# Kernel optimization log

Measured on AMD Instinct MI355X. Metric: run time of the kernel, lower is better.

## Reference

```python
import jax, jax.numpy as jnp
import numpy as np
from jax import lax

# Model constants (match init_kwargs)
DIM = 512
NUM_HEADS = 8
HEAD_DIM = 64
INNER = NUM_HEADS * HEAD_DIM  # 512
SCALE = HEAD_DIM ** -0.5
# CoaT ConvRelPosEnc window dict {3:2, 5:3, 7:3}: head-group sizes and kernel sizes
HEAD_SPLITS = [2, 3, 3]
KSIZES = [3, 5, 7]


def _depthwise_conv(x, w, b):
    # x: [B, Cg, H, W], w: [Cg, 1, k, k] (OIHW, depthwise), b: [Cg]
    cg = x.shape[1]
    y = lax.conv_general_dilated(
        x, w, window_strides=(1, 1), padding='SAME',
        feature_group_count=cg,
        dimension_numbers=('NCHW', 'OIHW', 'NCHW'))
    return y + b[None, :, None, None]


def setup_inputs() -> dict:
    key = jax.random.key(0)
    ks = jax.random.split(key, 10)
    B, Himg, Wimg = 16, 56, 56
    N = Himg * Wimg
    x = jax.random.normal(ks[0], (B, N, DIM), dtype=jnp.float32)
    w_qkv = jax.random.normal(ks[1], (3 * INNER, DIM), dtype=jnp.float32) * 0.02
    w_proj = jax.random.normal(ks[2], (DIM, INNER), dtype=jnp.float32) * 0.02
    b_proj = jnp.zeros((DIM,), dtype=jnp.float32)
    # depthwise conv params per head group: channels = split * HEAD_DIM
    w3 = jax.random.normal(ks[3], (2 * HEAD_DIM, 1, 3, 3), dtype=jnp.float32) * 0.02
    b3 = jnp.zeros((2 * HEAD_DIM,), dtype=jnp.float32)
    w5 = jax.random.normal(ks[4], (3 * HEAD_DIM, 1, 5, 5), dtype=jnp.float32) * 0.02
    b5 = jnp.zeros((3 * HEAD_DIM,), dtype=jnp.float32)
    w7 = jax.random.normal(ks[5], (3 * HEAD_DIM, 1, 7, 7), dtype=jnp.float32) * 0.02
    b7 = jnp.zeros((3 * HEAD_DIM,), dtype=jnp.float32)
    return {"x": x, "H": Himg, "W": Wimg,
            "w_qkv": w_qkv, "w_proj": w_proj, "b_proj": b_proj,
            "w3": w3, "b3": b3, "w5": w5, "b5": b5, "w7": w7, "b7": b7}


def reference(x, H, W, w_qkv, w_proj, b_proj, w3, b3, w5, b5, w7, b7):
    B, N, C = x.shape
    h, d = NUM_HEADS, HEAD_DIM
    qkv = x @ w_qkv.T  # [B, N, 3*INNER]
    q, k, v = jnp.split(qkv, 3, axis=-1)
    # b n (h d) -> b h n d
    def to_heads(t):
        return t.reshape(B, N, h, d).transpose(0, 2, 1, 3)
    q, k, v = to_heads(q), to_heads(k), to_heads(v)
    # factorized attention: softmax(k) over sequence dim, then two batched GEMMs
    k_softmax = jax.nn.softmax(k, axis=2)
    kv = jnp.einsum('bhnk,bhnv->bhkv', k_softmax, v)          # [B,h,d,d]
    factor_att = jnp.einsum('bhnk,bhkv->bhnv', q, kv)          # [B,h,N,d]
    # ConvRelPosEnc: depthwise conv on v (as 2D map), elementwise multiply by q
    v_img = v.transpose(0, 1, 3, 2).reshape(B, h * d, H, W)    # [B, h*d, H, W]
    c0, c1 = HEAD_SPLITS[0] * d, (HEAD_SPLITS[0] + HEAD_SPLITS[1]) * d
    conv_v = jnp.concatenate([
        _depthwise_conv(v_img[:, :c0], w3, b3),
        _depthwise_conv(v_img[:, c0:c1], w5, b5),
        _depthwise_conv(v_img[:, c1:], w7, b7),
    ], axis=1)                                                 # [B, h*d, H, W]
    conv_v = conv_v.reshape(B, h, d, N).transpose(0, 1, 3, 2)  # [B,h,N,d]
    crpe = q * conv_v
    out = SCALE * factor_att + crpe                            # [B,h,N,d]
    out = out.transpose(0, 2, 1, 3).reshape(B, N, h * d)       # b h n d -> b n (h d)
    out = out @ w_proj.T + b_proj
    return out
```

## Files before the change

### kernel.cpp

```cpp
#include <hip/hip_runtime.h>
#include <hip/hip_bf16.h>
#include <cstdint>
#include <cstddef>

using u16 = unsigned short;
using u32 = unsigned int;
using f32x4 = __attribute__((ext_vector_type(4))) float;
using bf16x8 = __attribute__((ext_vector_type(8))) short;

#define NB   16
#define NSEQ 3136
#define NH   8
#define HD   64
#define CDIM 512
#define CQKV 1536

static __device__ __forceinline__ u16 f2bf(float f) {
  u32 u = __builtin_bit_cast(u32, f);
  u = (u + 0x7FFFu + ((u >> 16) & 1u)) >> 16;
  return (u16)u;
}
static __device__ __forceinline__ float bf2f(u16 h) {
  u32 u = ((u32)h) << 16;
  return __builtin_bit_cast(float, u);
}
static __device__ __forceinline__ void async16(const void* g, void* l) {
  __builtin_amdgcn_global_load_lds((const __attribute__((address_space(1))) u32*)g,
                                   (__attribute__((address_space(3))) u32*)l, 16, 0, 0);
}

__global__ __launch_bounds__(256) void cvt_kernel(const float* __restrict__ in,
                                                  u16* __restrict__ out, int n4) {
  int i = (int)(blockIdx.x * 256 + threadIdx.x);
  if (i >= n4) return;
  f32x4 v = *(const f32x4*)(in + (size_t)i * 4);
  uint2 uu;
  uu.x = (u32)f2bf(v[0]) | ((u32)f2bf(v[1]) << 16);
  uu.y = (u32)f2bf(v[2]) | ((u32)f2bf(v[3]) << 16);
  *(uint2*)(out + (size_t)i * 4) = uu;
}

#define VMW(n) asm volatile("s_waitcnt vmcnt(" #n ")" ::: "memory")

template<bool OUT_FP32>
__global__ __launch_bounds__(512, 2) void gemm256(
    const u16* __restrict__ Ap, const u16* __restrict__ Bp, void* __restrict__ Cp,
    const float* __restrict__ bias, int K, int lda, int ldb, int ldc, int nbn)
{
  __shared__ u16 sm[2][2][2][128 * 64];
  int nwg = (int)gridDim.x;
  int bid = (int)blockIdx.x;
  int wg = (bid & 7) * (nwg >> 3) + (bid >> 3);
  int bm = wg / nbn, bn = wg - bm * nbn;
  int m0 = bm * 256, n0 = bn * 256;
  int t = (int)threadIdx.x;
  int lane = t & 63, w = t >> 6;
  int wm = w >> 2, wn = w & 3;
  int lr = lane & 15, lk = (lane >> 4) * 8;

  f32x4 acc[2][2][4][2] = {};
  bf16x8 av[4][2], bv[2][2];
  const int KT = K >> 6;

  auto stage = [&](int b, int op, int half, int kt) {
    const u16* P = op ? Bp : Ap;
    int ld = op ? ldb : lda;
    int base0 = op ? n0 : m0;
    int gc = (kt << 6) + ((((t & 7) ^ ((t >> 3) & 7))) << 3);
    #pragma unroll
    for (int rd = 0; rd < 2; ++rd) {
      int gr = base0 + half * 128 + rd * 64 + (t >> 3);
      async16(P + (size_t)gr * ld + gc, &sm[b][op][half][rd * 4096 + w * 512]);
    }
  };
  auto LOADA = [&](int b, int h) {
    #pragma unroll
    for (int mi = 0; mi < 4; ++mi)
      #pragma unroll
      for (int kk = 0; kk < 2; ++kk) {
        int r = wm * 64 + mi * 16 + lr;
        int c = kk * 32 + lk;
        av[mi][kk] = *(const bf16x8*)&sm[b][0][h][r * 64 + (c ^ ((r & 7) << 3))];
      }
  };
  auto LOADB = [&](int b, int g) {
    #pragma unroll
    for (int ni = 0; ni < 2; ++ni)
      #pragma unroll
      for (int kk = 0; kk < 2; ++kk) {
        int r = wn * 32 + ni * 16 + lr;
        int c = kk * 32 + lk;
        bv[ni][kk] = *(const bf16x8*)&sm[b][1][g][r * 64 + (c ^ ((r & 7) << 3))];
      }
  };

#define BARSEQ                                                  \
  __builtin_amdgcn_s_barrier();                                 \
  asm volatile("s_waitcnt lgkmcnt(0)" ::: "memory");            \
  __builtin_amdgcn_sched_barrier(0);                            \
  __builtin_amdgcn_s_setprio(1)
#define ENDP                                                    \
  __builtin_amdgcn_s_setprio(0);                                \
  __builtin_amdgcn_s_barrier()
#define MMQ(h_, g_)                                                          \
  _Pragma("unroll")                                                          \
  for (int kk = 0; kk < 2; ++kk) {                                           \
    _Pragma("unroll")                                                        \
    for (int mi = 0; mi < 4; ++mi) {                                         \
      _Pragma("unroll")                                                      \
      for (int ni = 0; ni < 2; ++ni)                                         \
        acc[h_][g_][mi][ni] = __builtin_amdgcn_mfma_f32_16x16x32_bf16(       \
            av[mi][kk], bv[ni][kk], acc[h_][g_][mi][ni], 0, 0, 0);           \
    }                                                                        \
  }

  stage(0, 0, 0, 0); stage(0, 1, 0, 0); stage(0, 0, 1, 0); stage(0, 1, 1, 0);
  VMW(4);
  __builtin_amdgcn_s_barrier();

  for (int kt = 0; kt < KT - 1; ++kt) {
    int bb = kt & 1;
    LOADA(bb, 0); LOADB(bb, 0);
    stage(bb ^ 1, 0, 0, kt + 1);
    VMW(2);
    BARSEQ; MMQ(0, 0); ENDP;
    LOADB(bb, 1);
    stage(bb ^ 1, 1, 0, kt + 1);
    BARSEQ; MMQ(0, 1); ENDP;
    LOADA(bb, 1);
    stage(bb ^ 1, 0, 1, kt + 1);
    BARSEQ; MMQ(1, 1); ENDP;
    LOADB(bb, 0);
    stage(bb ^ 1, 1, 1, kt + 1);
    VMW(4);
    BARSEQ; MMQ(1, 0); ENDP;
  }
  {
    int bb = (KT - 1) & 1;
    LOADA(bb, 0); LOADB(bb, 0);
    VMW(0);
    BARSEQ; MMQ(0, 0); ENDP;
    LOADB(bb, 1);
    BARSEQ; MMQ(0, 1); ENDP;
    LOADA(bb, 1);
    BARSEQ; MMQ(1, 1); ENDP;
    LOADB(bb, 0);
    BARSEQ; MMQ(1, 0); ENDP;
  }
#undef MMQ
#undef BARSEQ
#undef ENDP

  if constexpr (!OUT_FP32) {
    __syncthreads();
    u16* cs = (u16*)sm;
    #pragma unroll
    for (int h = 0; h < 2; ++h)
      #pragma unroll
      for (int g = 0; g < 2; ++g)
        #pragma unroll
        for (int mi = 0; mi < 4; ++mi)
          #pragma unroll
          for (int ni = 0; ni < 2; ++ni)
            #pragma unroll
            for (int r = 0; r < 4; ++r) {
              int row = h * 128 + wm * 64 + mi * 16 + (lane >> 4) * 4 + r;
              int col = g * 128 + wn * 32 + ni * 16 + lr;
              cs[row * 256 + (col ^ (((row >> 2) & 7) << 3))] = f2bf(acc[h][g][mi][ni][r]);
            }
    __syncthreads();
    #pragma unroll
    for (int i = 0; i < 16; ++i) {
      int e = (i * 512 + t) * 8;
      int row = e >> 8, col = e & 255;
      uint4 v = *(const uint4*)&cs[row * 256 + (col ^ (((row >> 2) & 7) << 3))];
      *(uint4*)&((u16*)Cp)[(size_t)(m0 + row) * ldc + n0 + col] = v;
    }
  } else {
    float* cf = (float*)sm;
    #pragma unroll
    for (int h = 0; h < 2; ++h) {
      __syncthreads();
      #pragma unroll
      for (int g = 0; g < 2; ++g)
        #pragma unroll
        for (int mi = 0; mi < 4; ++mi)
          #pragma unroll
          for (int ni = 0; ni < 2; ++ni)
            #pragma unroll
            for (int r = 0; r < 4; ++r) {
              int row = wm * 64 + mi * 16 + (lane >> 4) * 4 + r;
              int col = g * 128 + wn * 32 + ni * 16 + lr;
              cf[row * 256 + (col ^ (((row >> 2) & 7) << 3))] = acc[h][g][mi][ni][r];
            }
      __syncthreads();
      #pragma unroll
      for (int i = 0; i < 16; ++i) {
        int e = (i * 512 + t) * 4;
        int row = e >> 8, col = e & 255;
        f32x4 v = *(const f32x4*)&cf[row * 256 + (col ^ (((row >> 2) & 7) << 3))];
        f32x4 b4 = *(const f32x4*)&bias[n0 + col];
        v += b4;
        *(f32x4*)&((float*)Cp)[(size_t)(m0 + h * 128 + row) * ldc + n0 + col] = v;
      }
    }
  }
}


static __device__ __forceinline__ void kvp_body(int bid, char* smem,
    const u16* __restrict__ qkvb, float* __restrict__ part) {
  int ns = bid & 7, h = (bid >> 3) & 7, b = bid >> 6;
  int t = (int)threadIdx.x;
  int lane = t & 63, w = t >> 6;
  float* ek = (float*)smem;
  u16*  vv  = (u16*)(smem + 14336);
  float* mg = (float*)(smem + 21504);
  int dk0 = (lane >> 3) * 8, dv0 = (lane & 7) * 8;
  float acc[8][8] = {};
  float sacc = 0.f;
  int nbase = ns * 392;
  for (int c0 = 0; c0 < 392; c0 += 56) {
    __syncthreads();
    for (int idx = t; idx < 448; idx += 256) {
      int row = idx >> 3, c8 = idx & 7;
      size_t go = (size_t)(b * NSEQ + nbase + c0 + row) * CQKV + h * HD + c8 * 8;
      uint4 kq = *(const uint4*)&qkvb[go + CDIM];
      uint4 vq = *(const uint4*)&qkvb[go + 2 * CDIM];
      const u16* kp = (const u16*)&kq;
      #pragma unroll
      for (int j = 0; j < 8; ++j)
        ek[row * 64 + c8 * 8 + j] = __expf(bf2f(kp[j]));
      *(uint4*)&vv[row * 64 + c8 * 8] = vq;
    }
    __syncthreads();
    if (w == 0) {
      #pragma unroll 4
      for (int n = 0; n < 56; ++n) sacc += ek[n * 64 + lane];
    }
    for (int n = w * 14; n < w * 14 + 14; ++n) {
      f32x4 e0 = *(const f32x4*)&ek[n * 64 + dk0];
      f32x4 e1 = *(const f32x4*)&ek[n * 64 + dk0 + 4];
      bf16x8 vq = *(const bf16x8*)&vv[n * 64 + dv0];
      float vf[8];
      #pragma unroll
      for (int j = 0; j < 8; ++j) vf[j] = bf2f((u16)vq[j]);
      #pragma unroll
      for (int i = 0; i < 4; ++i)
        #pragma unroll
        for (int j = 0; j < 8; ++j) {
          acc[i][j]     += e0[i] * vf[j];
          acc[i + 4][j] += e1[i] * vf[j];
        }
    }
  }
  __syncthreads();
  for (int wi = 0; wi < 4; ++wi) {
    if (w == wi) {
      #pragma unroll
      for (int i = 0; i < 8; ++i) {
        #pragma unroll
        for (int j4 = 0; j4 < 2; ++j4) {
          f32x4* p = (f32x4*)&mg[(dk0 + i) * 64 + dv0 + j4 * 4];
          f32x4 a;
          #pragma unroll
          for (int j = 0; j < 4; ++j) a[j] = acc[i][j4 * 4 + j];
          if (wi == 0) *p = a; else *p += a;
        }
      }
    }
    __syncthreads();
  }
  float* dst = part + (size_t)((ns * 16 + b) * 8 + h) * 4160;
  for (int i4 = t; i4 < 1024; i4 += 256)
    *(f32x4*)&dst[i4 * 4] = *(const f32x4*)&mg[i4 * 4];
  if (w == 0) dst[4096 + lane] = sacc;
}

template<int R>
static __device__ __forceinline__ void conv_body(int bid, char* smem,
    const u16* __restrict__ qkvb, u16* __restrict__ cvout,
    const float* __restrict__ wp, const float* __restrict__ bias, int hbase, int nh) {
  constexpr int KS = 2 * R + 1;
  constexpr int WT = 14 + 2 * R;
  u16* vt = (u16*)smem;
  int hh = bid % nh;
  int tile = (bid / nh) & 15;
  int b = bid / (nh * 16);
  int h = hbase + hh;
  int y0 = (tile >> 2) * 14, x0 = (tile & 3) * 14;
  int t = (int)threadIdx.x;
  for (int idx = t; idx < WT * WT * 8; idx += 256) {
    int pix = idx >> 3, c8 = idx & 7;
    int py = pix / WT, px = pix - py * WT;
    int gy = y0 + py - R, gx = x0 + px - R;
    uint4 val; val.x = 0u; val.y = 0u; val.z = 0u; val.w = 0u;
    if (gy >= 0 && gy < 56 && gx >= 0 && gx < 56)
      val = *(const uint4*)&qkvb[(size_t)(b * NSEQ + gy * 56 + gx) * CQKV + 2 * CDIM + h * HD + c8 * 8];
    *(uint4*)&vt[pix * 64 + c8 * 8] = val;
  }
  __syncthreads();
  int d = t & 63, g = t >> 6;
  int cg = hh * 64 + d;
  float wr[KS * KS];
  #pragma unroll
  for (int i = 0; i < KS * KS; ++i) wr[i] = wp[cg * KS * KS + i];
  float bb = bias[cg];
  for (int px = g; px < 14; px += 4) {
    float acc[14];
    #pragma unroll
    for (int i = 0; i < 14; ++i) acc[i] = bb;
    #pragma unroll
    for (int iy = 0; iy < 14 + 2 * R; ++iy) {
      float val[KS];
      #pragma unroll
      for (int dx = 0; dx < KS; ++dx) val[dx] = bf2f(vt[(iy * WT + px + dx) * 64 + d]);
      #pragma unroll
      for (int dy = 0; dy < KS; ++dy) {
        int py = iy - dy;
        if (py >= 0 && py < 14) {
          #pragma unroll
          for (int dx = 0; dx < KS; ++dx) acc[py] += wr[dy * KS + dx] * val[dx];
        }
      }
    }
    #pragma unroll
    for (int py = 0; py < 14; ++py)
      cvout[(size_t)(b * NSEQ + (y0 + py) * 56 + x0 + px) * CDIM + h * HD + d] = f2bf(acc[py]);
  }
}

__global__ __launch_bounds__(256) void mid_kernel(const u16* __restrict__ qkvb,
    u16* __restrict__ cvout, float* __restrict__ part,
    const float* __restrict__ w3, const float* __restrict__ b3,
    const float* __restrict__ w5, const float* __restrict__ b5,
    const float* __restrict__ w7, const float* __restrict__ b7) {
  __shared__ alignas(16) char smem[51200];
  int bid = (int)blockIdx.x;
  int q3 = bid / 3, r3 = bid - q3 * 3;
  if (r3 == 0) {
    kvp_body(q3, smem, qkvb, part);
  } else {
    int cid = 2 * q3 + (r3 - 1);
    if (cid < 512)        conv_body<1>(cid,        smem, qkvb, cvout, w3, b3, 0, 2);
    else if (cid < 1280)  conv_body<2>(cid - 512,  smem, qkvb, cvout, w5, b5, 2, 3);
    else                  conv_body<3>(cid - 1280, smem, qkvb, cvout, w7, b7, 5, 3);
  }
}

__global__ __launch_bounds__(256) void kv_reduce_kernel(const float* __restrict__ part,
                                                        float* __restrict__ kvb) {
  int idx = (int)(blockIdx.x * 256 + threadIdx.x);
  int bh = idx >> 10, e4 = idx & 1023;
  int b = bh >> 3, h = bh & 7;
  int dk = e4 >> 4;
  float s = 0.f;
  f32x4 o; o[0] = 0.f; o[1] = 0.f; o[2] = 0.f; o[3] = 0.f;
  #pragma unroll
  for (int c = 0; c < 8; ++c) {
    const float* src = part + (size_t)((c * 16 + b) * 8 + h) * 4160;
    o += *(const f32x4*)&src[e4 * 4];
    s += src[4096 + dk];
  }
  float inv = 1.0f / s;
  o *= inv;
  *(f32x4*)&kvb[(size_t)bh * 4096 + e4 * 4] = o;
}

__global__ __launch_bounds__(256) void combine_kernel(u16* __restrict__ qkvb,
                                                      const u16* __restrict__ cvin,
                                                      const float* __restrict__ kvb) {
  int bid = (int)blockIdx.x;
  int rt = bid % 49;
  int h = (bid / 49) & 7;
  int b = bid / 392;
  int n0 = rt * 64;
  int t = (int)threadIdx.x;
  int lane = t & 63, w = t >> 6;
  __shared__ u16 qs[64 * 72];
  __shared__ u16 cvs[64 * 64];
  __shared__ u16 kvT[64 * 64];

  #pragma unroll
  for (int i = 0; i < 2; ++i) {
    int idx = i * 256 + t;
    int row = idx >> 3, c8 = idx & 7;
    int srccol = (c8 ^ (row & 7)) << 3;
    async16(qkvb + (size_t)(b * NSEQ + n0 + row) * CQKV + h * HD + srccol, &qs[idx * 8]);
    async16(cvin + (size_t)(b * NSEQ + n0 + row) * CDIM + h * HD + srccol, &cvs[idx * 8]);
  }
  const float* kvsrc = kvb + (size_t)(b * 8 + h) * 4096;
  #pragma unroll
  for (int i = 0; i < 4; ++i) {
    int idx = i * 256 + t;
    int dk = idx & 63, dv0 = (idx >> 6) * 4;
    f32x4 v = *(const f32x4*)&kvsrc[dk * 64 + dv0];
    #pragma unroll
    for (int j = 0; j < 4; ++j) {
      int dv = dv0 + j;
      kvT[dv * 64 + ((((dk >> 3) ^ (dv & 7)) << 3) | (dk & 7))] = f2bf(v[j]);
    }
  }
  VMW(0);
  __syncthreads();

  int lr = lane & 15, lk = (lane >> 4) * 8;
  f32x4 acc[4] = {};
  bf16x8 av[2], bv[4][2];
  #pragma unroll
  for (int kk = 0; kk < 2; ++kk) {
    int r = w * 16 + lr;
    int c = kk * 32 + lk;
    av[kk] = *(const bf16x8*)&qs[r * 64 + (c ^ ((r & 7) << 3))];
  }
  #pragma unroll
  for (int ni = 0; ni < 4; ++ni)
    #pragma unroll
    for (int kk = 0; kk < 2; ++kk) {
      int r = ni * 16 + lr;
      int c = kk * 32 + lk;
      bv[ni][kk] = *(const bf16x8*)&kvT[r * 64 + (c ^ ((r & 7) << 3))];
    }
  #pragma unroll
  for (int kk = 0; kk < 2; ++kk)
    #pragma unroll
    for (int ni = 0; ni < 4; ++ni)
      acc[ni] = __builtin_amdgcn_mfma_f32_16x16x32_bf16(av[kk], bv[ni][kk], acc[ni], 0, 0, 0);

  float outv[4][4];
  #pragma unroll
  for (int ni = 0; ni < 4; ++ni)
    #pragma unroll
    for (int r = 0; r < 4; ++r) {
      int nrow = w * 16 + (lane >> 4) * 4 + r;
      int dv = ni * 16 + lr;
      int sw = ((((dv >> 3) ^ (nrow & 7)) << 3) | (dv & 7));
      float qv = bf2f(qs[nrow * 64 + sw]);
      float cv = bf2f(cvs[nrow * 64 + sw]);
      outv[ni][r] = 0.125f * acc[ni][r] + qv * cv;
    }
  __syncthreads();
  #pragma unroll
  for (int ni = 0; ni < 4; ++ni)
    #pragma unroll
    for (int r = 0; r < 4; ++r) {
      int nrow = w * 16 + (lane >> 4) * 4 + r;
      int dv = ni * 16 + lr;
      qs[nrow * 72 + dv] = f2bf(outv[ni][r]);
    }
  __syncthreads();
  {
    int row = t >> 2, c0 = (t & 3) * 16;
    uint4 x0 = *(const uint4*)&qs[row * 72 + c0];
    uint4 x1 = *(const uint4*)&qs[row * 72 + c0 + 8];
    u16* dst = &qkvb[(size_t)(b * NSEQ + n0 + row) * CQKV + h * HD + c0];
    *(uint4*)dst = x0;
    *(uint4*)&dst[8] = x1;
  }
}

extern "C" void kernel_launch(void* const* d_in, const int* in_sizes, int n_in,
                              void* d_out, int out_size, void* d_ws, size_t ws_size,
                              hipStream_t stream) {
  (void)in_sizes; (void)n_in; (void)out_size; (void)ws_size;
  const float* x      = (const float*)d_in[0];
  const float* w_qkv  = (const float*)d_in[3];
  const float* w_proj = (const float*)d_in[4];
  const float* b_proj = (const float*)d_in[5];
  const float* w3 = (const float*)d_in[6];
  const float* b3 = (const float*)d_in[7];
  const float* w5 = (const float*)d_in[8];
  const float* b5 = (const float*)d_in[9];
  const float* w7 = (const float*)d_in[10];
  const float* b7 = (const float*)d_in[11];
  float* out = (float*)d_out;

  char* ws = (char*)d_ws;
  u16* qkvb = (u16*)ws;        ws += (size_t)50176 * 1536 * 2;
  u16* wqb  = (u16*)ws;        ws += (size_t)1536 * 512 * 2;
  u16* wpb  = (u16*)ws;        ws += (size_t)512 * 512 * 2;
  float* kvpart = (float*)ws;  ws += (size_t)1024 * 4160 * 4;
  float* kvb = (float*)ws;     ws += (size_t)16 * 8 * 64 * 64 * 4;
  u16* xb = (u16*)ws;          ws += (size_t)50176 * 512 * 2;

  cvt_kernel<<<768, 256, 0, stream>>>(w_qkv, wqb, 1536 * 512 / 4);
  cvt_kernel<<<256, 256, 0, stream>>>(w_proj, wpb, 512 * 512 / 4);
  cvt_kernel<<<25088, 256, 0, stream>>>(x, xb, 50176 * 512 / 4);
  gemm256<false><<<1176, 512, 0, stream>>>(xb, wqb, qkvb, nullptr,
                                           512, 512, 512, 1536, 6);
  mid_kernel<<<3072, 256, 0, stream>>>(qkvb, xb, kvpart, w3, b3, w5, b5, w7, b7);
  kv_reduce_kernel<<<512, 256, 0, stream>>>(kvpart, kvb);
  combine_kernel<<<6272, 256, 0, stream>>>(qkvb, xb, kvb);
  gemm256<true><<<392, 512, 0, stream>>>(qkvb, wpb, out, b_proj,
                                         512, 1536, 512, 512, 2);
}
```

Before: 310.2 us.

## Compute KV partial outer products with bf16 MFMA instead of scalar FMAs

The softmax-numerator times V accumulation in the kvp stage is rewritten to stage exp(k) and v transposed into swizzled LDS tiles of 64 tokens and run 16x16x32 bf16 MFMA instructions. Each wave now owns 16 rows of the 64x64 result, which removes the cross-wave LDS reduction loop and its barriers, and the column sums are computed from the same tile with lane shuffles. The cost is that exp(k) is rounded to bf16 before the matrix multiply and the sum, which lowers precision. The last tile is partial and is zero-padded.

```diff
diff --git a/kernel.cpp b/kernel.cpp
--- a/kernel.cpp
+++ b/kernel.cpp
@@ -213,68 +213,79 @@
   int ns = bid & 7, h = (bid >> 3) & 7, b = bid >> 6;
   int t = (int)threadIdx.x;
   int lane = t & 63, w = t >> 6;
-  float* ek = (float*)smem;
-  u16*  vv  = (u16*)(smem + 14336);
-  float* mg = (float*)(smem + 21504);
-  int dk0 = (lane >> 3) * 8, dv0 = (lane & 7) * 8;
-  float acc[8][8] = {};
+  u16* ekT = (u16*)smem;
+  u16* vT  = (u16*)(smem + 8192);
+  int nbase = ns * 392;
+  int lr = lane & 15, lg = lane >> 4;
+  f32x4 acc[4] = {};
   float sacc = 0.f;
-  int nbase = ns * 392;
-  for (int c0 = 0; c0 < 392; c0 += 56) {
+
+  for (int tile = 0; tile < 7; ++tile) {
     __syncthreads();
-    for (int idx = t; idx < 448; idx += 256) {
-      int row = idx >> 3, c8 = idx & 7;
-      size_t go = (size_t)(b * NSEQ + nbase + c0 + row) * CQKV + h * HD + c8 * 8;
-      uint4 kq = *(const uint4*)&qkvb[go + CDIM];
-      uint4 vq = *(const uint4*)&qkvb[go + 2 * CDIM];
+    int lim = 392 - tile * 64;
+    #pragma unroll
+    for (int it = 0; it < 2; ++it) {
+      int idx = it * 256 + t;
+      int n = idx >> 3, c8 = idx & 7;
+      uint4 kq; kq.x = 0u; kq.y = 0u; kq.z = 0u; kq.w = 0u;
+      uint4 vq = kq;
+      bool ok = (n < lim);
+      if (ok) {
+        size_t go = (size_t)(b * NSEQ + nbase + tile * 64 + n) * CQKV + h * HD + c8 * 8;
+        kq = *(const uint4*)&qkvb[go + CDIM];
+        vq = *(const uint4*)&qkvb[go + 2 * CDIM];
+      }
       const u16* kp = (const u16*)&kq;
-      #pragma unroll
-      for (int j = 0; j < 8; ++j)
-        ek[row * 64 + c8 * 8 + j] = __expf(bf2f(kp[j]));
-      *(uint4*)&vv[row * 64 + c8 * 8] = vq;
+      const u16* vp = (const u16*)&vq;
+      #pragma unroll
+      for (int j = 0; j < 8; ++j) {
+        int d = c8 * 8 + j;
+        int pc = n ^ ((d & 7) << 3);
+        ekT[d * 64 + pc] = ok ? f2bf(__expf(bf2f(kp[j]))) : (u16)0;
+        vT [d * 64 + pc] = vp[j];
+      }
     }
     __syncthreads();
-    if (w == 0) {
-      #pragma unroll 4
-      for (int n = 0; n < 56; ++n) sacc += ek[n * 64 + lane];
-    }
-    for (int n = w * 14; n < w * 14 + 14; ++n) {
-      f32x4 e0 = *(const f32x4*)&ek[n * 64 + dk0];
-      f32x4 e1 = *(const f32x4*)&ek[n * 64 + dk0 + 4];
-      bf16x8 vq = *(const bf16x8*)&vv[n * 64 + dv0];
-      float vf[8];
-      #pragma unroll
-      for (int j = 0; j < 8; ++j) vf[j] = bf2f((u16)vq[j]);
-      #pragma unroll
-      for (int i = 0; i < 4; ++i)
-        #pragma unroll
-        for (int j = 0; j < 8; ++j) {
-          acc[i][j]     += e0[i] * vf[j];
-          acc[i + 4][j] += e1[i] * vf[j];
-        }
-    }
-  }
-  __syncthreads();
-  for (int wi = 0; wi < 4; ++wi) {
-    if (w == wi) {
-      #pragma unroll
-      for (int i = 0; i < 8; ++i) {
-        #pragma unroll
-        for (int j4 = 0; j4 < 2; ++j4) {
-          f32x4* p = (f32x4*)&mg[(dk0 + i) * 64 + dv0 + j4 * 4];
-          f32x4 a;
-          #pragma unroll
-          for (int j = 0; j < 4; ++j) a[j] = acc[i][j4 * 4 + j];
-          if (wi == 0) *p = a; else *p += a;
-        }
-      }
-    }
-    __syncthreads();
-  }
+    bf16x8 av[2], bv[4][2];
+    #pragma unroll
+    for (int kk = 0; kk < 2; ++kk) {
+      int r = w * 16 + lr;
+      int c = kk * 32 + lg * 8;
+      av[kk] = *(const bf16x8*)&ekT[r * 64 + (c ^ ((r & 7) << 3))];
+    }
+    #pragma unroll
+    for (int ni = 0; ni < 4; ++ni)
+      #pragma unroll
+      for (int kk = 0; kk < 2; ++kk) {
+        int r = ni * 16 + lr;
+        int c = kk * 32 + lg * 8;
+        bv[ni][kk] = *(const bf16x8*)&vT[r * 64 + (c ^ ((r & 7) << 3))];
+      }
+    #pragma unroll
+    for (int kk = 0; kk < 2; ++kk)
+      #pragma unroll
+      for (int ni = 0; ni < 4; ++ni)
+        acc[ni] = __builtin_amdgcn_mfma_f32_16x16x32_bf16(av[kk], bv[ni][kk], acc[ni], 0, 0, 0);
+    {
+      int r = w * 16 + lr;
+      int c0 = lg * 16;
+      bf16x8 s0 = *(const bf16x8*)&ekT[r * 64 + (c0 ^ ((r & 7) << 3))];
+      bf16x8 s1 = *(const bf16x8*)&ekT[r * 64 + ((c0 + 8) ^ ((r & 7) << 3))];
+      float ss = 0.f;
+      #pragma unroll
+      for (int j = 0; j < 8; ++j) ss += bf2f((u16)s0[j]) + bf2f((u16)s1[j]);
+      sacc += ss;
+    }
+  }
+  sacc += __shfl_xor(sacc, 16, 64);
+  sacc += __shfl_xor(sacc, 32, 64);
   float* dst = part + (size_t)((ns * 16 + b) * 8 + h) * 4160;
-  for (int i4 = t; i4 < 1024; i4 += 256)
-    *(f32x4*)&dst[i4 * 4] = *(const f32x4*)&mg[i4 * 4];
-  if (w == 0) dst[4096 + lane] = sacc;
+  #pragma unroll
+  for (int ni = 0; ni < 4; ++ni)
+    #pragma unroll
+    for (int r = 0; r < 4; ++r)
+      dst[(w * 16 + lg * 4 + r) * 64 + ni * 16 + lr] = acc[ni][r];
+  if (lane < 16) dst[4096 + w * 16 + lane] = sacc;
 }
 
 template<int R>
```

Measured after the change: 312.7 us. About the same (+0.8%).
